# Performance work log

Hardware: AMD Instinct MI355X
Metric: run time of the kernel (lower is better)

## Reference

```python
import jax, jax.numpy as jnp
import numpy as np

DIM = 256
KEY_DIM = 16
NUM_HEADS = 8
ATTN_RATIO = 4
NH_KD = KEY_DIM * NUM_HEADS   # 128
D = ATTN_RATIO * KEY_DIM      # 64
DH = D * NUM_HEADS            # 512
POS_LEN = 16
SCALE = KEY_DIM ** -0.5


def _cbn(x, w, s, b):
    # 1x1 conv (no bias) + folded BatchNorm affine. w: [out,in], x: [B,in,H,W]
    y = jnp.einsum('oi,bihw->bohw', w, x)
    return y * s[None, :, None, None] + b[None, :, None, None]


def _interp_pos(pos, n):
    # F.interpolate(mode='linear', align_corners=False) from length POS_LEN to n.
    L = pos.shape[-1]
    coords = (jnp.arange(n, dtype=pos.dtype) + 0.5) * (L / n) - 0.5
    coords = jnp.clip(coords, 0.0, L - 1)
    lo = jnp.floor(coords).astype(jnp.int32)
    hi = jnp.minimum(lo + 1, L - 1)
    t = coords - lo.astype(pos.dtype)
    return pos[..., lo] * (1 - t) + pos[..., hi] * t  # [1,C,n]


def _axial_attn(q_emb, k_emb, v_emb, pos_q, pos_k, n):
    # q_emb/k_emb: [B,NH_KD,n], v_emb: [B,DH,n]
    B = q_emb.shape[0]
    q = (q_emb + _interp_pos(pos_q, n)).reshape(B, NUM_HEADS, KEY_DIM, n)
    k = (k_emb + _interp_pos(pos_k, n)).reshape(B, NUM_HEADS, KEY_DIM, n)
    v = v_emb.reshape(B, NUM_HEADS, D, n)
    attn = jnp.einsum('bhcn,bhcm->bhnm', q, k) * SCALE
    attn = jax.nn.softmax(attn, axis=-1)
    xx = jnp.einsum('bhnm,bhdm->bhnd', attn, v)      # [B,NH,n,D]
    return xx.transpose(0, 1, 3, 2).reshape(B, DH, n)  # [B,DH,n]


def _forward(x, wq, sq, bq, wk, sk, bk, wv, sv, bv,
             pos_rowq, pos_rowk, pos_colq, pos_colk,
             w_row, s_row, b_row, w_col, s_col, b_col,
             w_proj, s_proj, b_proj, w_sc, s_sc, b_sc,
             w_dw, s_dw, b_dw, w_pw, s_pw, b_pw):
    B, C, H, W = x.shape
    q = _cbn(x, wq, sq, bq)   # [B,NH_KD,H,W]
    k = _cbn(x, wk, sk, bk)
    v = _cbn(x, wv, sv, bv)   # [B,DH,H,W]

    # row branch (mean over W)
    xx_row = _axial_attn(q.mean(-1), k.mean(-1), v.mean(-1), pos_rowq, pos_rowk, H)
    xx_row = _cbn(jax.nn.relu(xx_row[..., None]), w_row, s_row, b_row)      # [B,DH,H,1]
    # column branch (mean over H)
    xx_col = _axial_attn(q.mean(-2), k.mean(-2), v.mean(-2), pos_colq, pos_colk, W)
    xx_col = _cbn(jax.nn.relu(xx_col[:, :, None, :]), w_col, s_col, b_col)  # [B,DH,1,W]

    attn_out = v + (xx_row + xx_col)
    attn_out = _cbn(jax.nn.relu(attn_out), w_proj, s_proj, b_proj)          # [B,DIM,H,W]

    # gate branch: 1x1 -> dw3x3 -> relu -> 1x1 -> h_sigmoid
    gate = _cbn(x, w_sc, s_sc, b_sc)
    gate = jax.lax.conv_general_dilated(
        gate, w_dw, (1, 1), 'SAME',
        dimension_numbers=('NCHW', 'OIHW', 'NCHW'), feature_group_count=DIM)
    gate = gate * s_dw[None, :, None, None] + b_dw[None, :, None, None]
    gate = jax.nn.relu(gate)
    gate = _cbn(gate, w_pw, s_pw, b_pw)
    gate = jnp.clip(gate + 3.0, 0.0, 6.0) / 6.0  # h_sigmoid
    return gate * attn_out


def setup_inputs() -> dict:
    key = jax.random.key(0)
    ks = jax.random.split(key, 32)
    B, H, W = 16, 64, 64
    nrm = lambda k, sh, sc=0.05: jax.random.normal(k, sh, dtype=jnp.float32) * sc
    inp = {
        'x': nrm(ks[0], (B, DIM, H, W), 1.0),
        'wq': nrm(ks[1], (NH_KD, DIM)), 'sq': 1.0 + nrm(ks[2], (NH_KD,)), 'bq': nrm(ks[3], (NH_KD,)),
        'wk': nrm(ks[4], (NH_KD, DIM)), 'sk': 1.0 + nrm(ks[5], (NH_KD,)), 'bk': nrm(ks[6], (NH_KD,)),
        'wv': nrm(ks[7], (DH, DIM)), 'sv': 1.0 + nrm(ks[8], (DH,)), 'bv': nrm(ks[9], (DH,)),
        'pos_rowq': nrm(ks[10], (1, NH_KD, POS_LEN), 1.0), 'pos_rowk': nrm(ks[11], (1, NH_KD, POS_LEN), 1.0),
        'pos_colq': nrm(ks[12], (1, NH_KD, POS_LEN), 1.0), 'pos_colk': nrm(ks[13], (1, NH_KD, POS_LEN), 1.0),
        'w_row': nrm(ks[14], (DH, DH)), 's_row': 1.0 + nrm(ks[15], (DH,)), 'b_row': nrm(ks[16], (DH,)),
        'w_col': nrm(ks[17], (DH, DH)), 's_col': 1.0 + nrm(ks[18], (DH,)), 'b_col': nrm(ks[19], (DH,)),
        'w_proj': nrm(ks[20], (DIM, DH)), 's_proj': 1.0 + nrm(ks[21], (DIM,)), 'b_proj': nrm(ks[22], (DIM,)),
        'w_sc': nrm(ks[23], (DIM, DIM)), 's_sc': 1.0 + nrm(ks[24], (DIM,)), 'b_sc': nrm(ks[25], (DIM,)),
        'w_dw': nrm(ks[26], (DIM, 1, 3, 3)), 's_dw': 1.0 + nrm(ks[27], (DIM,)), 'b_dw': nrm(ks[28], (DIM,)),
        'w_pw': nrm(ks[29], (DIM, DIM)), 's_pw': 1.0 + nrm(ks[30], (DIM,)), 'b_pw': nrm(ks[31], (DIM,)),
    }
    return inp


def reference(x, wq, sq, bq, wk, sk, bk, wv, sv, bv,
              pos_rowq, pos_rowk, pos_colq, pos_colk,
              w_row, s_row, b_row, w_col, s_col, b_col,
              w_proj, s_proj, b_proj, w_sc, s_sc, b_sc,
              w_dw, s_dw, b_dw, w_pw, s_pw, b_pw):
    return _forward(x, wq, sq, bq, wk, sk, bk, wv, sv, bv,
                    pos_rowq, pos_rowk, pos_colq, pos_colk,
                    w_row, s_row, b_row, w_col, s_col, b_col,
                    w_proj, s_proj, b_proj, w_sc, s_sc, b_sc,
                    w_dw, s_dw, b_dw, w_pw, s_pw, b_pw)
```

## Files before the change

kernel.cpp:

```cpp
#include <hip/hip_runtime.h>
#include <math.h>

typedef unsigned short u16;
typedef unsigned int u32;
typedef short short8 __attribute__((ext_vector_type(8)));
typedef float f32x4 __attribute__((ext_vector_type(4)));

#define Bn 16
#define Cc 256
#define Pp 4096
#define DHc 512
#define PTOT 65536
#define SCALE 0.25f

__device__ __forceinline__ float bf2f(u16 u) {
    return __uint_as_float(((u32)u) << 16);
}
__device__ __forceinline__ u16 f2bf(float f) {
    u32 u = __float_as_uint(f);
    u32 lsb = (u >> 16) & 1u;
    u += 0x7fffu + lsb;
    return (u16)(u >> 16);
}

__device__ __forceinline__ void gload16(const u16* g, u16* l) {
    __builtin_amdgcn_global_load_lds(
        (const __attribute__((address_space(1))) void*)(uintptr_t)g,
        (__attribute__((address_space(3))) void*)(u32)(uintptr_t)l,
        16, 0, 0);
}

__global__ __launch_bounds__(256) void mean_kernel(
    const float* __restrict__ x, u16* __restrict__ xmb) {
    __shared__ float plane[64][65];
    int bc = blockIdx.x;
    int b = bc >> 8, c = bc & 255;
    const float* xp = x + (size_t)bc * Pp;
    int tid = threadIdx.x;
#pragma unroll
    for (int k = 0; k < 16; ++k) {
        int idx = tid + k * 256;
        plane[idx >> 6][idx & 63] = xp[idx];
    }
    __syncthreads();
    if (tid < 64) {
        float s = 0.f;
#pragma unroll
        for (int w = 0; w < 64; ++w) s += plane[tid][w];
        xmb[((size_t)b * 64 + tid) * 256 + c] = f2bf(s * (1.f / 64.f));
    } else if (tid < 128) {
        int w = tid - 64;
        float s = 0.f;
#pragma unroll
        for (int h = 0; h < 64; ++h) s += plane[h][w];
        xmb[((size_t)1024 + b * 64 + w) * 256 + c] = f2bf(s * (1.f / 64.f));
    }
}

__global__ __launch_bounds__(256) void xpose_kernel(
    const float* __restrict__ x, u16* __restrict__ xbf) {
    __shared__ float tile[64][65];
    int pb = blockIdx.x;
    int cb = blockIdx.y;
    int b = blockIdx.z;
    int t = threadIdx.x;
    int p_l = t & 63, c_q = t >> 6;
    const float* xp = x + ((size_t)b * Cc + cb * 64) * Pp + pb * 64;
#pragma unroll
    for (int rr = 0; rr < 16; ++rr) {
        int c_l = rr * 4 + c_q;
        tile[p_l][c_l] = xp[(size_t)c_l * Pp + p_l];
    }
    __syncthreads();
    int c_l2 = t & 63, p_q = t >> 6;
    u16* dst = xbf + ((size_t)b * Pp + pb * 64) * Cc + cb * 64;
#pragma unroll
    for (int rr = 0; rr < 16; ++rr) {
        int p_l2 = rr * 4 + p_q;
        dst[(size_t)p_l2 * Cc + c_l2] = f2bf(tile[p_l2][c_l2]);
    }
}

__global__ __launch_bounds__(256) void wconv_kernel(
    const float* __restrict__ wq, const float* __restrict__ wk, const float* __restrict__ wv,
    const float* __restrict__ wsc, const float* __restrict__ wproj, const float* __restrict__ wpw,
    const float* __restrict__ wrow, const float* __restrict__ wcol,
    const float* __restrict__ wdw,
    u16* __restrict__ wqkvb, u16* __restrict__ wscb,
    u16* __restrict__ wprojb, u16* __restrict__ wpwb,
    u16* __restrict__ wrb, u16* __restrict__ wcb, float* __restrict__ wdwT) {
    int t = blockIdx.x * 256 + threadIdx.x;
    if (t < 2304) wdwT[(t % 9) * 256 + (t / 9)] = wdw[t];
    if (t < 32768) wqkvb[t] = f2bf(wq[t]);
    else if (t < 65536) wqkvb[t] = f2bf(wk[t - 32768]);
    else if (t < 196608) wqkvb[t] = f2bf(wv[t - 65536]);
    else if (t < 262144) wscb[t - 196608] = f2bf(wsc[t - 196608]);
    else if (t < 393216) wprojb[t - 262144] = f2bf(wproj[t - 262144]);
    else if (t < 458752) wpwb[t - 393216] = f2bf(wpw[t - 393216]);
    else if (t < 720896) wrb[t - 458752] = f2bf(wrow[t - 458752]);
    else wcb[t - 720896] = f2bf(wcol[t - 720896]);
}

__device__ __forceinline__ void gemm_mainloop(
    const u16* __restrict__ W, const u16* __restrict__ X, int K,
    int o0, size_t prow0, u16* ldsA, u16* ldsB, f32x4 (&acc)[4][4]) {
    int t = threadIdx.x;
    int w = t >> 6, lane = t & 63;
    int sr = (w << 5) + (lane >> 2);
    int ks = (lane & 3) * 8;
    const u16* gA = W + (size_t)(o0 + sr) * K + ks;
    const u16* gB = X + (prow0 + sr) * K + ks;
    u16* lA = ldsA + sr * 32 + ks;
    u16* lB = ldsB + sr * 32 + ks;
    int wo = (w >> 1) * 64, wp = (w & 1) * 64;
    const u16* fA = ldsA + (wo + (lane & 15)) * 32 + ((lane >> 4) * 8);
    const u16* fB = ldsB + (wp + (lane & 15)) * 32 + ((lane >> 4) * 8);

    for (int k0 = 0; k0 < K; k0 += 32) {
        if (k0) __syncthreads();
        gload16(gA + k0, lA);
        gload16(gA + k0 + (size_t)16 * K, lA + 16 * 32);
        gload16(gB + k0, lB);
        gload16(gB + k0 + (size_t)16 * K, lB + 16 * 32);
        __syncthreads();
        short8 a[4], b[4];
#pragma unroll
        for (int i = 0; i < 4; ++i) a[i] = *(const short8*)(fA + i * 16 * 32);
#pragma unroll
        for (int j = 0; j < 4; ++j) b[j] = *(const short8*)(fB + j * 16 * 32);
#pragma unroll
        for (int i = 0; i < 4; ++i)
#pragma unroll
            for (int j = 0; j < 4; ++j)
                acc[i][j] = __builtin_amdgcn_mfma_f32_16x16x32_bf16(a[i], b[j], acc[i][j], 0, 0, 0);
    }
}

__global__ __launch_bounds__(256) void gemm_qkv(
    const u16* __restrict__ Wb, const u16* __restrict__ X,
    const float* __restrict__ sq, const float* __restrict__ bq,
    const float* __restrict__ sk, const float* __restrict__ bk,
    const float* __restrict__ sv, const float* __restrict__ bv,
    const float* __restrict__ posrq, const float* __restrict__ posrk,
    const float* __restrict__ poscq, const float* __restrict__ posck,
    float* __restrict__ qrow, float* __restrict__ krow, float* __restrict__ vrow,
    float* __restrict__ qcol, float* __restrict__ kcol, float* __restrict__ vcol) {
    __shared__ u16 ldsA[128 * 32];
    __shared__ u16 ldsB[128 * 32];
    f32x4 acc[4][4];
#pragma unroll
    for (int i = 0; i < 4; ++i)
#pragma unroll
        for (int j = 0; j < 4; ++j) acc[i][j] = (f32x4){0.f, 0.f, 0.f, 0.f};
    int o0 = blockIdx.x * 128;
    size_t prow0 = (size_t)blockIdx.y * 128;
    gemm_mainloop(Wb, X, 256, o0, prow0, ldsA, ldsB, acc);

    int lane = threadIdx.x & 63, w = threadIdx.x >> 6;
    int wo = (w >> 1) * 64, wp = (w & 1) * 64;
    int quad = lane >> 4, cn = lane & 15;
#pragma unroll
    for (int j = 0; j < 4; ++j) {
        int p = (int)prow0 + wp + j * 16 + cn;
        int branch = p >> 10, loc = p & 1023;
        int b = loc >> 6, n = loc & 63;
        float coords = 0.25f * (float)n - 0.375f;
        coords = fminf(fmaxf(coords, 0.f), 15.f);
        int lo = (int)floorf(coords);
        int hi = min(lo + 1, 15);
        float tt = coords - (float)lo;
#pragma unroll
        for (int i = 0; i < 4; ++i) {
            int o = o0 + wo + i * 16 + quad * 4;
            if (o < 128) {
                const float* pos = branch ? poscq : posrq;
                float* dst = branch ? qcol : qrow;
#pragma unroll
                for (int r = 0; r < 4; ++r) {
                    int c = o + r;
                    float pv = pos[c * 16 + lo] * (1.f - tt) + pos[c * 16 + hi] * tt;
                    dst[b * 8192 + c * 64 + n] = acc[i][j][r] * sq[c] + bq[c] + pv;
                }
            } else if (o < 256) {
                const float* pos = branch ? posck : posrk;
                float* dst = branch ? kcol : krow;
#pragma unroll
                for (int r = 0; r < 4; ++r) {
                    int c = o - 128 + r;
                    float pv = pos[c * 16 + lo] * (1.f - tt) + pos[c * 16 + hi] * tt;
                    dst[b * 8192 + c * 64 + n] = acc[i][j][r] * sk[c] + bk[c] + pv;
                }
            } else {
                float* dst = branch ? vcol : vrow;
#pragma unroll
                for (int r = 0; r < 4; ++r) {
                    int c = o - 256 + r;
                    dst[b * 32768 + c * 64 + n] = acc[i][j][r] * sv[c] + bv[c];
                }
            }
        }
    }
}

__global__ __launch_bounds__(512) void attn_kernel(
    const float* __restrict__ qr, const float* __restrict__ kr, const float* __restrict__ vr,
    const float* __restrict__ qc, const float* __restrict__ kc, const float* __restrict__ vc,
    u16* __restrict__ xxbf) {
    int branch = blockIdx.y;
    const float* q = branch ? qc : qr;
    const float* k = branch ? kc : kr;
    const float* v = branch ? vc : vr;
    int bh = blockIdx.x;
    int b = bh >> 3, h = bh & 7;
    __shared__ float qs[16][64], ks[16][64], vs[64][64];
    int t = threadIdx.x;
#pragma unroll
    for (int i = t; i < 1024; i += 512) {
        int c = i >> 6, nn = i & 63;
        qs[c][nn] = q[b * 8192 + (h * 16 + c) * 64 + nn];
        ks[c][nn] = k[b * 8192 + (h * 16 + c) * 64 + nn];
    }
#pragma unroll
    for (int i = t; i < 4096; i += 512) {
        int d = i >> 6, nn = i & 63;
        vs[d][nn] = v[b * 32768 + (h * 64 + d) * 64 + nn];
    }
    __syncthreads();

    int n = t & 63, dq = t >> 6;
    float qv[16];
#pragma unroll
    for (int c = 0; c < 16; ++c) qv[c] = qs[c][n];

    float s[64];
    float mx = -1e30f;
    for (int m = 0; m < 64; ++m) {
        float acc = 0.f;
#pragma unroll
        for (int c = 0; c < 16; ++c) acc += qv[c] * ks[c][m];
        acc *= SCALE;
        s[m] = acc;
        mx = fmaxf(mx, acc);
    }
    float sum = 0.f;
    for (int m = 0; m < 64; ++m) {
        s[m] = __expf(s[m] - mx);
        sum += s[m];
    }
    float inv = 1.f / sum;
    u16* dst = xxbf + (((size_t)(b * 2 + branch)) * 64 + n) * 512 + h * 64 + dq * 8;
#pragma unroll
    for (int dd = 0; dd < 8; ++dd) {
        int d = dq * 8 + dd;
        float acc = 0.f;
#pragma unroll 8
        for (int m = 0; m < 64; ++m) acc += s[m] * vs[d][m];
        dst[dd] = f2bf(fmaxf(acc * inv, 0.f));
    }
}

__global__ __launch_bounds__(256) void post_gemm(
    const u16* __restrict__ xxbf, const u16* __restrict__ wrb, const u16* __restrict__ wcb,
    const float* __restrict__ s_row, const float* __restrict__ b_row,
    const float* __restrict__ s_col, const float* __restrict__ b_col,
    float* __restrict__ xr2, float* __restrict__ xc2) {
    __shared__ u16 ldsA[64 * 32];
    __shared__ u16 ldsB[256 * 32];
    int o0 = blockIdx.x * 256;
    int b = blockIdx.y;
    int branch = blockIdx.z;
    const u16* A = xxbf + ((size_t)(b * 2 + branch)) * 64 * 512;
    const u16* W = branch ? wcb : wrb;
    const float* ss = branch ? s_col : s_row;
    const float* bb = branch ? b_col : b_row;
    float* dst = (branch ? xc2 : xr2) + (size_t)b * 32768;

    f32x4 acc[4][4];
#pragma unroll
    for (int i = 0; i < 4; ++i)
#pragma unroll
        for (int j = 0; j < 4; ++j) acc[i][j] = (f32x4){0.f, 0.f, 0.f, 0.f};

    int t = threadIdx.x, w = t >> 6, lane = t & 63;
    int ks = (t & 3) * 8;
    const u16* gA = A + (size_t)(t >> 2) * 512 + ks;
    const u16* gB = W + (size_t)(o0 + (t >> 2)) * 512 + ks;
    u16* lA = ldsA + (t >> 2) * 32 + ks;
    u16* lB = ldsB + (t >> 2) * 32 + ks;
    const u16* fA = ldsA + (lane & 15) * 32 + ((lane >> 4) * 8);
    const u16* fB = ldsB + (w * 64 + (lane & 15)) * 32 + ((lane >> 4) * 8);

    for (int k0 = 0; k0 < 512; k0 += 32) {
        if (k0) __syncthreads();
        gload16(gA + k0, lA);
#pragma unroll
        for (int r = 0; r < 4; ++r)
            gload16(gB + k0 + (size_t)r * 64 * 512, lB + r * 64 * 32);
        __syncthreads();
        short8 a[4], bfr[4];
#pragma unroll
        for (int i = 0; i < 4; ++i) a[i] = *(const short8*)(fA + i * 16 * 32);
#pragma unroll
        for (int j = 0; j < 4; ++j) bfr[j] = *(const short8*)(fB + j * 16 * 32);
#pragma unroll
        for (int i = 0; i < 4; ++i)
#pragma unroll
            for (int j = 0; j < 4; ++j)
                acc[i][j] = __builtin_amdgcn_mfma_f32_16x16x32_bf16(a[i], bfr[j], acc[i][j], 0, 0, 0);
    }

    int quad = lane >> 4, cn = lane & 15;
#pragma unroll
    for (int i = 0; i < 4; ++i)
#pragma unroll
        for (int j = 0; j < 4; ++j) {
            int o = o0 + w * 64 + j * 16 + cn;
            float sv_ = ss[o], bv_ = bb[o];
#pragma unroll
            for (int r = 0; r < 4; ++r) {
                int n = i * 16 + quad * 4 + r;
                dst[n * 512 + o] = acc[i][j][r] * sv_ + bv_;
            }
        }
}

__global__ __launch_bounds__(256) void gemm_sc(
    const u16* __restrict__ Wb, const u16* __restrict__ X,
    const float* __restrict__ s, const float* __restrict__ bb, u16* __restrict__ outb) {
    __shared__ u16 ldsA[128 * 32];
    __shared__ u16 ldsB[128 * 32];
    f32x4 acc[4][4];
#pragma unroll
    for (int i = 0; i < 4; ++i)
#pragma unroll
        for (int j = 0; j < 4; ++j) acc[i][j] = (f32x4){0.f, 0.f, 0.f, 0.f};
    int o0 = blockIdx.x * 128;
    size_t prow0 = (size_t)blockIdx.y * 128;
    gemm_mainloop(Wb, X, 256, o0, prow0, ldsA, ldsB, acc);

    int lane = threadIdx.x & 63, w = threadIdx.x >> 6;
    int wo = (w >> 1) * 64, wp = (w & 1) * 64;
    int quad = lane >> 4, cn = lane & 15;
#pragma unroll
    for (int i = 0; i < 4; ++i) {
        int ob = o0 + wo + i * 16 + quad * 4;
        f32x4 s4 = *(const f32x4*)&s[ob];
        f32x4 b4 = *(const f32x4*)&bb[ob];
#pragma unroll
        for (int j = 0; j < 4; ++j) {
            size_t p = prow0 + wp + j * 16 + cn;
            ushort4 o4;
            o4.x = f2bf(acc[i][j][0] * s4[0] + b4[0]);
            o4.y = f2bf(acc[i][j][1] * s4[1] + b4[1]);
            o4.z = f2bf(acc[i][j][2] * s4[2] + b4[2]);
            o4.w = f2bf(acc[i][j][3] * s4[3] + b4[3]);
            *(ushort4*)&outb[p * 256 + ob] = o4;
        }
    }
}

__global__ __launch_bounds__(256) void gemm_pw(
    const u16* __restrict__ Wb, const u16* __restrict__ X,
    const float* __restrict__ s, const float* __restrict__ bb, u16* __restrict__ outb) {
    __shared__ u16 ldsA[128 * 32];
    __shared__ u16 ldsB[128 * 32];
    f32x4 acc[4][4];
#pragma unroll
    for (int i = 0; i < 4; ++i)
#pragma unroll
        for (int j = 0; j < 4; ++j) acc[i][j] = (f32x4){0.f, 0.f, 0.f, 0.f};
    int o0 = blockIdx.x * 128;
    size_t prow0 = (size_t)blockIdx.y * 128;
    gemm_mainloop(Wb, X, 256, o0, prow0, ldsA, ldsB, acc);

    int lane = threadIdx.x & 63, w = threadIdx.x >> 6;
    int wo = (w >> 1) * 64, wp = (w & 1) * 64;
    int quad = lane >> 4, cn = lane & 15;
#pragma unroll
    for (int i = 0; i < 4; ++i) {
        int ob = o0 + wo + i * 16 + quad * 4;
        f32x4 s4 = *(const f32x4*)&s[ob];
        f32x4 b4 = *(const f32x4*)&bb[ob];
#pragma unroll
        for (int j = 0; j < 4; ++j) {
            size_t p = prow0 + wp + j * 16 + cn;
            ushort4 o4;
            o4.x = f2bf(fminf(fmaxf(acc[i][j][0] * s4[0] + b4[0] + 3.f, 0.f), 6.f) * (1.f / 6.f));
            o4.y = f2bf(fminf(fmaxf(acc[i][j][1] * s4[1] + b4[1] + 3.f, 0.f), 6.f) * (1.f / 6.f));
            o4.z = f2bf(fminf(fmaxf(acc[i][j][2] * s4[2] + b4[2] + 3.f, 0.f), 6.f) * (1.f / 6.f));
            o4.w = f2bf(fminf(fmaxf(acc[i][j][3] * s4[3] + b4[3] + 3.f, 0.f), 6.f) * (1.f / 6.f));
            *(ushort4*)&outb[p * 256 + ob] = o4;
        }
    }
}

__global__ __launch_bounds__(512, 4) void fused_vproj(
    const u16* __restrict__ Wv, const u16* __restrict__ Wp,
    const u16* __restrict__ X,
    const float* __restrict__ sv, const float* __restrict__ bv,
    const float* __restrict__ xr2, const float* __restrict__ xc2,
    const float* __restrict__ sp, const float* __restrict__ bp,
    const u16* __restrict__ gate, float* __restrict__ out) {
    __shared__ u16 lds[64 * 512];

    int t = threadIdx.x;
    int lane = t & 63, w = t >> 6;
    int quad = lane >> 4, cn = lane & 15;
    int ppx = cn & 7;
    int p0 = blockIdx.x * 64;
    int bi = p0 >> 12;
    int hh = (p0 >> 6) & 63;

#pragma unroll
    for (int r = 0; r < 4; ++r) {
        int li = r * 512 + t;
        int p = li >> 5, ko = li & 31;
        gload16(X + ((size_t)(p0 + p)) * 256 + ((ko ^ (p & 7)) << 3),
                lds + (size_t)li * 8);
    }
    __syncthreads();

    f32x4 acc1[4][4];
#pragma unroll
    for (int i = 0; i < 4; ++i)
#pragma unroll
        for (int j = 0; j < 4; ++j) acc1[i][j] = (f32x4){0.f, 0.f, 0.f, 0.f};

    int ow = w * 64;
    const u16* gA0 = Wv + (size_t)(ow + cn) * 256 + quad * 8;
    const u16* gA1 = gA0 + (size_t)16 * 256;
    const u16* gA2 = gA0 + (size_t)32 * 256;
    const u16* gA3 = gA0 + (size_t)48 * 256;

    for (int k0 = 0; k0 < 256; k0 += 32) {
        int og = (k0 >> 3) + quad;
        short8 a[4], b[4];
        a[0] = *(const short8*)(gA0 + k0);
        a[1] = *(const short8*)(gA1 + k0);
        a[2] = *(const short8*)(gA2 + k0);
        a[3] = *(const short8*)(gA3 + k0);
#pragma unroll
        for (int j = 0; j < 4; ++j) {
            int pl = j * 16 + cn;
            b[j] = *(const short8*)&lds[pl * 256 + ((og ^ ppx) << 3)];
        }
#pragma unroll
        for (int i = 0; i < 4; ++i)
#pragma unroll
            for (int j = 0; j < 4; ++j)
                acc1[i][j] = __builtin_amdgcn_mfma_f32_16x16x32_bf16(a[i], b[j], acc1[i][j], 0, 0, 0);
    }

    __syncthreads();

#pragma unroll
    for (int i = 0; i < 4; ++i) {
        int ob = ow + i * 16 + quad * 4;
        f32x4 s4 = *(const f32x4*)&sv[ob];
        f32x4 b4 = *(const f32x4*)&bv[ob];
        f32x4 ra = *(const f32x4*)&xr2[(size_t)bi * 32768 + hh * 512 + ob];
#pragma unroll
        for (int j = 0; j < 4; ++j) {
            int p = j * 16 + cn;
            f32x4 ca = *(const f32x4*)&xc2[(size_t)bi * 32768 + p * 512 + ob];
            ushort4 o4;
            o4.x = f2bf(fmaxf(acc1[i][j][0] * s4[0] + b4[0] + ra[0] + ca[0], 0.f));
            o4.y = f2bf(fmaxf(acc1[i][j][1] * s4[1] + b4[1] + ra[1] + ca[1], 0.f));
            o4.z = f2bf(fmaxf(acc1[i][j][2] * s4[2] + b4[2] + ra[2] + ca[2], 0.f));
            o4.w = f2bf(fmaxf(acc1[i][j][3] * s4[3] + b4[3] + ra[3] + ca[3], 0.f));
            *(ushort4*)&lds[p * 512 + (ob ^ ((p & 7) << 3))] = o4;
        }
    }
    __syncthreads();

    f32x4 acc2[2][4];
#pragma unroll
    for (int i = 0; i < 2; ++i)
#pragma unroll
        for (int j = 0; j < 4; ++j) acc2[i][j] = (f32x4){0.f, 0.f, 0.f, 0.f};

    int o2w = w * 32;
    const u16* gP0 = Wp + (size_t)(o2w + cn) * 512 + quad * 8;
    const u16* gP1 = gP0 + (size_t)16 * 512;

    for (int k0 = 0; k0 < 512; k0 += 32) {
        short8 a2[2], b2[4];
        a2[0] = *(const short8*)(gP0 + k0);
        a2[1] = *(const short8*)(gP1 + k0);
        int kk = k0 + quad * 8;
#pragma unroll
        for (int j = 0; j < 4; ++j) {
            int p = j * 16 + cn;
            b2[j] = *(const short8*)&lds[p * 512 + (kk ^ ((p & 7) << 3))];
        }
#pragma unroll
        for (int i = 0; i < 2; ++i)
#pragma unroll
            for (int j = 0; j < 4; ++j)
                acc2[i][j] = __builtin_amdgcn_mfma_f32_16x16x32_bf16(a2[i], b2[j], acc2[i][j], 0, 0, 0);
    }

    int pl0 = p0 & 4095;
#pragma unroll
    for (int i = 0; i < 2; ++i) {
        int ob = o2w + i * 16 + quad * 4;
        f32x4 s4 = *(const f32x4*)&sp[ob];
        f32x4 b4 = *(const f32x4*)&bp[ob];
#pragma unroll
        for (int j = 0; j < 4; ++j) {
            int p = j * 16 + cn;
            size_t pg = (size_t)p0 + p;
            ushort4 gv = *(const ushort4*)&gate[pg * 256 + ob];
            float* op = out + (size_t)bi * 1048576 + (size_t)ob * 4096 + (pl0 + p);
            op[0 * 4096] = bf2f(gv.x) * (acc2[i][j][0] * s4[0] + b4[0]);
            op[1 * 4096] = bf2f(gv.y) * (acc2[i][j][1] * s4[1] + b4[1]);
            op[2 * 4096] = bf2f(gv.z) * (acc2[i][j][2] * s4[2] + b4[2]);
            op[3 * 4096] = bf2f(gv.w) * (acc2[i][j][3] * s4[3] + b4[3]);
        }
    }
}

__global__ __launch_bounds__(256) void dw_kernel(
    const u16* __restrict__ sc, const float* __restrict__ wdwT,
    const float* __restrict__ sdw, const float* __restrict__ bdw, u16* __restrict__ dwout) {
    int t = blockIdx.x * 256 + threadIdx.x;
    int cg = (t & 31) * 8;
    size_t p = (size_t)(t >> 5);
    int h = (int)((p >> 6) & 63), w_ = (int)(p & 63);
    float acc[8] = {0.f, 0.f, 0.f, 0.f, 0.f, 0.f, 0.f, 0.f};
#pragma unroll
    for (int ky = 0; ky < 3; ++ky) {
        int hh = h + ky - 1;
        if (hh < 0 || hh > 63) continue;
#pragma unroll
        for (int kx = 0; kx < 3; ++kx) {
            int wx = w_ + kx - 1;
            if (wx < 0 || wx > 63) continue;
            size_t pp = (size_t)((long long)p + (ky - 1) * 64 + (kx - 1));
            short8 v = *(const short8*)&sc[pp * 256 + cg];
            const float* wt = &wdwT[(ky * 3 + kx) * 256 + cg];
            f32x4 w0 = *(const f32x4*)wt;
            f32x4 w1 = *(const f32x4*)(wt + 4);
            acc[0] += w0[0] * bf2f((u16)v[0]); acc[1] += w0[1] * bf2f((u16)v[1]);
            acc[2] += w0[2] * bf2f((u16)v[2]); acc[3] += w0[3] * bf2f((u16)v[3]);
            acc[4] += w1[0] * bf2f((u16)v[4]); acc[5] += w1[1] * bf2f((u16)v[5]);
            acc[6] += w1[2] * bf2f((u16)v[6]); acc[7] += w1[3] * bf2f((u16)v[7]);
        }
    }
    f32x4 s0 = *(const f32x4*)&sdw[cg], s1 = *(const f32x4*)&sdw[cg + 4];
    f32x4 b0 = *(const f32x4*)&bdw[cg], b1 = *(const f32x4*)&bdw[cg + 4];
    short8 o;
    o[0] = (short)f2bf(fmaxf(acc[0] * s0[0] + b0[0], 0.f));
    o[1] = (short)f2bf(fmaxf(acc[1] * s0[1] + b0[1], 0.f));
    o[2] = (short)f2bf(fmaxf(acc[2] * s0[2] + b0[2], 0.f));
    o[3] = (short)f2bf(fmaxf(acc[3] * s0[3] + b0[3], 0.f));
    o[4] = (short)f2bf(fmaxf(acc[4] * s1[0] + b1[0], 0.f));
    o[5] = (short)f2bf(fmaxf(acc[5] * s1[1] + b1[1], 0.f));
    o[6] = (short)f2bf(fmaxf(acc[6] * s1[2] + b1[2], 0.f));
    o[7] = (short)f2bf(fmaxf(acc[7] * s1[3] + b1[3], 0.f));
    *(short8*)&dwout[p * 256 + cg] = o;
}

extern "C" void kernel_launch(void* const* d_in, const int* in_sizes, int n_in,
                              void* d_out, int out_size, void* d_ws, size_t ws_size,
                              hipStream_t stream) {
    const float* x = (const float*)d_in[0];
    const float* wq = (const float*)d_in[1];
    const float* sq = (const float*)d_in[2];
    const float* bq = (const float*)d_in[3];
    const float* wk = (const float*)d_in[4];
    const float* sk = (const float*)d_in[5];
    const float* bk = (const float*)d_in[6];
    const float* wv = (const float*)d_in[7];
    const float* sv = (const float*)d_in[8];
    const float* bv = (const float*)d_in[9];
    const float* posrq = (const float*)d_in[10];
    const float* posrk = (const float*)d_in[11];
    const float* poscq = (const float*)d_in[12];
    const float* posck = (const float*)d_in[13];
    const float* w_row = (const float*)d_in[14];
    const float* s_row = (const float*)d_in[15];
    const float* b_row = (const float*)d_in[16];
    const float* w_col = (const float*)d_in[17];
    const float* s_col = (const float*)d_in[18];
    const float* b_col = (const float*)d_in[19];
    const float* w_proj = (const float*)d_in[20];
    const float* s_proj = (const float*)d_in[21];
    const float* b_proj = (const float*)d_in[22];
    const float* w_sc = (const float*)d_in[23];
    const float* s_sc = (const float*)d_in[24];
    const float* b_sc = (const float*)d_in[25];
    const float* w_dw = (const float*)d_in[26];
    const float* s_dw = (const float*)d_in[27];
    const float* b_dw = (const float*)d_in[28];
    const float* w_pw = (const float*)d_in[29];
    const float* s_pw = (const float*)d_in[30];
    const float* b_pw = (const float*)d_in[31];
    float* out = (float*)d_out;

    float* fws = (float*)d_ws;
    float* qrow = fws;
    float* krow = qrow + 131072;
    float* qcol = krow + 131072;
    float* kcol = qcol + 131072;
    float* vrow = kcol + 131072;
    float* vcol = vrow + 524288;
    float* xr2  = vcol + 524288;
    float* xc2  = xr2 + 524288;
    float* wdwT = xc2 + 524288;
    u16* xmb    = (u16*)(wdwT + 2304);
    u16* xbf    = xmb + 524288;
    u16* wqkvb  = xbf + (size_t)PTOT * 256;
    u16* wscb   = wqkvb + 196608;
    u16* wprojb = wscb + 65536;
    u16* wpwb   = wprojb + 131072;
    u16* wrb    = wpwb + 65536;
    u16* wcb    = wrb + 262144;
    u16* xxbf   = wcb + 262144;
    u16* scb    = xxbf + 1048576;
    u16* dwb    = scb + (size_t)PTOT * 256;
    u16* gate   = scb;

    mean_kernel<<<dim3(Bn * Cc), 256, 0, stream>>>(x, xmb);
    xpose_kernel<<<dim3(64, 4, Bn), 256, 0, stream>>>(x, xbf);
    wconv_kernel<<<dim3(3840), 256, 0, stream>>>(
        wq, wk, wv, w_sc, w_proj, w_pw, w_row, w_col, w_dw,
        wqkvb, wscb, wprojb, wpwb, wrb, wcb, wdwT);
    gemm_qkv<<<dim3(6, 16), 256, 0, stream>>>(
        wqkvb, xmb, sq, bq, sk, bk, sv, bv,
        posrq, posrk, poscq, posck, qrow, krow, vrow, qcol, kcol, vcol);
    attn_kernel<<<dim3(128, 2), 512, 0, stream>>>(qrow, krow, vrow, qcol, kcol, vcol, xxbf);
    post_gemm<<<dim3(2, Bn, 2), 256, 0, stream>>>(
        xxbf, wrb, wcb, s_row, b_row, s_col, b_col, xr2, xc2);
    gemm_sc<<<dim3(2, 512), 256, 0, stream>>>(wscb, xbf, s_sc, b_sc, scb);
    dw_kernel<<<dim3(8192), 256, 0, stream>>>(scb, wdwT, s_dw, b_dw, dwb);
    gemm_pw<<<dim3(2, 512), 256, 0, stream>>>(wpwb, dwb, s_pw, b_pw, gate);
    fused_vproj<<<dim3(1024), 512, 0, stream>>>(
        wqkvb + 65536, wprojb, xbf, sv, bv, xr2, xc2, s_proj, b_proj, gate, out);
}
```

Baseline: 460.6 us.

## Shrink GEMM tiles to 32 pixels and load operands directly from global memory

Merges the shortcut and pointwise 1x1-conv GEMMs into one kernel that takes a hard-sigmoid flag. That kernel uses 512-thread blocks over 32-pixel tiles and reads A and B fragments straight from global memory instead of staging them through LDS. The fused v/proj kernel likewise halves its pixel tile to 32, drops the LDS staging of X, and launches twice as many blocks. The aim is more parallelism and less LDS and barrier overhead, at the cost of less operand reuse per block and more redundant global and L2 traffic for the weights.

```diff
diff --git a/kernel.cpp b/kernel.cpp
--- a/kernel.cpp
+++ b/kernel.cpp
@@ -324,71 +324,59 @@
         }
 }
 
-__global__ __launch_bounds__(256) void gemm_sc(
+__global__ __launch_bounds__(512, 4) void gemm_cbn256(
     const u16* __restrict__ Wb, const u16* __restrict__ X,
-    const float* __restrict__ s, const float* __restrict__ bb, u16* __restrict__ outb) {
-    __shared__ u16 ldsA[128 * 32];
-    __shared__ u16 ldsB[128 * 32];
-    f32x4 acc[4][4];
-#pragma unroll
-    for (int i = 0; i < 4; ++i)
-#pragma unroll
-        for (int j = 0; j < 4; ++j) acc[i][j] = (f32x4){0.f, 0.f, 0.f, 0.f};
-    int o0 = blockIdx.x * 128;
-    size_t prow0 = (size_t)blockIdx.y * 128;
-    gemm_mainloop(Wb, X, 256, o0, prow0, ldsA, ldsB, acc);
-
-    int lane = threadIdx.x & 63, w = threadIdx.x >> 6;
-    int wo = (w >> 1) * 64, wp = (w & 1) * 64;
+    const float* __restrict__ s, const float* __restrict__ bb,
+    u16* __restrict__ outb, int hsig) {
+    int t = threadIdx.x;
+    int lane = t & 63, w = t >> 6;
     int quad = lane >> 4, cn = lane & 15;
-#pragma unroll
-    for (int i = 0; i < 4; ++i) {
-        int ob = o0 + wo + i * 16 + quad * 4;
+    size_t p0 = (size_t)blockIdx.x * 32;
+    int o2w = w * 32;
+
+    const u16* gA0 = Wb + (size_t)(o2w + cn) * 256 + quad * 8;
+    const u16* gA1 = gA0 + (size_t)16 * 256;
+    const u16* gB0 = X + (p0 + cn) * 256 + quad * 8;
+    const u16* gB1 = gB0 + (size_t)16 * 256;
+
+    f32x4 acc[2][2];
+#pragma unroll
+    for (int i = 0; i < 2; ++i)
+#pragma unroll
+        for (int j = 0; j < 2; ++j) acc[i][j] = (f32x4){0.f, 0.f, 0.f, 0.f};
+
+#pragma unroll
+    for (int k0 = 0; k0 < 256; k0 += 32) {
+        short8 a0 = *(const short8*)(gA0 + k0);
+        short8 a1 = *(const short8*)(gA1 + k0);
+        short8 b0 = *(const short8*)(gB0 + k0);
+        short8 b1 = *(const short8*)(gB1 + k0);
+        acc[0][0] = __builtin_amdgcn_mfma_f32_16x16x32_bf16(a0, b0, acc[0][0], 0, 0, 0);
+        acc[0][1] = __builtin_amdgcn_mfma_f32_16x16x32_bf16(a0, b1, acc[0][1], 0, 0, 0);
+        acc[1][0] = __builtin_amdgcn_mfma_f32_16x16x32_bf16(a1, b0, acc[1][0], 0, 0, 0);
+        acc[1][1] = __builtin_amdgcn_mfma_f32_16x16x32_bf16(a1, b1, acc[1][1], 0, 0, 0);
+    }
+
+#pragma unroll
+    for (int i = 0; i < 2; ++i) {
+        int ob = o2w + i * 16 + quad * 4;
         f32x4 s4 = *(const f32x4*)&s[ob];
         f32x4 b4 = *(const f32x4*)&bb[ob];
 #pragma unroll
-        for (int j = 0; j < 4; ++j) {
-            size_t p = prow0 + wp + j * 16 + cn;
+        for (int j = 0; j < 2; ++j) {
+            size_t p = p0 + j * 16 + cn;
             ushort4 o4;
-            o4.x = f2bf(acc[i][j][0] * s4[0] + b4[0]);
-            o4.y = f2bf(acc[i][j][1] * s4[1] + b4[1]);
-            o4.z = f2bf(acc[i][j][2] * s4[2] + b4[2]);
-            o4.w = f2bf(acc[i][j][3] * s4[3] + b4[3]);
-            *(ushort4*)&outb[p * 256 + ob] = o4;
-        }
-    }
-}
-
-__global__ __launch_bounds__(256) void gemm_pw(
-    const u16* __restrict__ Wb, const u16* __restrict__ X,
-    const float* __restrict__ s, const float* __restrict__ bb, u16* __restrict__ outb) {
-    __shared__ u16 ldsA[128 * 32];
-    __shared__ u16 ldsB[128 * 32];
-    f32x4 acc[4][4];
-#pragma unroll
-    for (int i = 0; i < 4; ++i)
-#pragma unroll
-        for (int j = 0; j < 4; ++j) acc[i][j] = (f32x4){0.f, 0.f, 0.f, 0.f};
-    int o0 = blockIdx.x * 128;
-    size_t prow0 = (size_t)blockIdx.y * 128;
-    gemm_mainloop(Wb, X, 256, o0, prow0, ldsA, ldsB, acc);
-
-    int lane = threadIdx.x & 63, w = threadIdx.x >> 6;
-    int wo = (w >> 1) * 64, wp = (w & 1) * 64;
-    int quad = lane >> 4, cn = lane & 15;
-#pragma unroll
-    for (int i = 0; i < 4; ++i) {
-        int ob = o0 + wo + i * 16 + quad * 4;
-        f32x4 s4 = *(const f32x4*)&s[ob];
-        f32x4 b4 = *(const f32x4*)&bb[ob];
-#pragma unroll
-        for (int j = 0; j < 4; ++j) {
-            size_t p = prow0 + wp + j * 16 + cn;
-            ushort4 o4;
-            o4.x = f2bf(fminf(fmaxf(acc[i][j][0] * s4[0] + b4[0] + 3.f, 0.f), 6.f) * (1.f / 6.f));
-            o4.y = f2bf(fminf(fmaxf(acc[i][j][1] * s4[1] + b4[1] + 3.f, 0.f), 6.f) * (1.f / 6.f));
-            o4.z = f2bf(fminf(fmaxf(acc[i][j][2] * s4[2] + b4[2] + 3.f, 0.f), 6.f) * (1.f / 6.f));
-            o4.w = f2bf(fminf(fmaxf(acc[i][j][3] * s4[3] + b4[3] + 3.f, 0.f), 6.f) * (1.f / 6.f));
+            if (hsig) {
+                o4.x = f2bf(fminf(fmaxf(acc[i][j][0] * s4[0] + b4[0] + 3.f, 0.f), 6.f) * (1.f / 6.f));
+                o4.y = f2bf(fminf(fmaxf(acc[i][j][1] * s4[1] + b4[1] + 3.f, 0.f), 6.f) * (1.f / 6.f));
+                o4.z = f2bf(fminf(fmaxf(acc[i][j][2] * s4[2] + b4[2] + 3.f, 0.f), 6.f) * (1.f / 6.f));
+                o4.w = f2bf(fminf(fmaxf(acc[i][j][3] * s4[3] + b4[3] + 3.f, 0.f), 6.f) * (1.f / 6.f));
+            } else {
+                o4.x = f2bf(acc[i][j][0] * s4[0] + b4[0]);
+                o4.y = f2bf(acc[i][j][1] * s4[1] + b4[1]);
+                o4.z = f2bf(acc[i][j][2] * s4[2] + b4[2]);
+                o4.w = f2bf(acc[i][j][3] * s4[3] + b4[3]);
+            }
             *(ushort4*)&outb[p * 256 + ob] = o4;
         }
     }
@@ -401,57 +389,39 @@
     const float* __restrict__ xr2, const float* __restrict__ xc2,
     const float* __restrict__ sp, const float* __restrict__ bp,
     const u16* __restrict__ gate, float* __restrict__ out) {
-    __shared__ u16 lds[64 * 512];
+    __shared__ u16 abt[32 * 512];
 
     int t = threadIdx.x;
     int lane = t & 63, w = t >> 6;
     int quad = lane >> 4, cn = lane & 15;
-    int ppx = cn & 7;
-    int p0 = blockIdx.x * 64;
+    int p0 = blockIdx.x * 32;
     int bi = p0 >> 12;
     int hh = (p0 >> 6) & 63;
-
-#pragma unroll
-    for (int r = 0; r < 4; ++r) {
-        int li = r * 512 + t;
-        int p = li >> 5, ko = li & 31;
-        gload16(X + ((size_t)(p0 + p)) * 256 + ((ko ^ (p & 7)) << 3),
-                lds + (size_t)li * 8);
-    }
-    __syncthreads();
-
-    f32x4 acc1[4][4];
+    int w0 = p0 & 63;
+
+    f32x4 acc1[4][2];
 #pragma unroll
     for (int i = 0; i < 4; ++i)
 #pragma unroll
-        for (int j = 0; j < 4; ++j) acc1[i][j] = (f32x4){0.f, 0.f, 0.f, 0.f};
+        for (int j = 0; j < 2; ++j) acc1[i][j] = (f32x4){0.f, 0.f, 0.f, 0.f};
 
     int ow = w * 64;
-    const u16* gA0 = Wv + (size_t)(ow + cn) * 256 + quad * 8;
-    const u16* gA1 = gA0 + (size_t)16 * 256;
-    const u16* gA2 = gA0 + (size_t)32 * 256;
-    const u16* gA3 = gA0 + (size_t)48 * 256;
-
+    const u16* gA = Wv + (size_t)(ow + cn) * 256 + quad * 8;
+    const u16* gB = X + ((size_t)p0 + cn) * 256 + quad * 8;
+
+#pragma unroll
     for (int k0 = 0; k0 < 256; k0 += 32) {
-        int og = (k0 >> 3) + quad;
-        short8 a[4], b[4];
-        a[0] = *(const short8*)(gA0 + k0);
-        a[1] = *(const short8*)(gA1 + k0);
-        a[2] = *(const short8*)(gA2 + k0);
-        a[3] = *(const short8*)(gA3 + k0);
-#pragma unroll
-        for (int j = 0; j < 4; ++j) {
-            int pl = j * 16 + cn;
-            b[j] = *(const short8*)&lds[pl * 256 + ((og ^ ppx) << 3)];
-        }
+        short8 a[4], b[2];
+#pragma unroll
+        for (int i = 0; i < 4; ++i) a[i] = *(const short8*)(gA + (size_t)i * 16 * 256 + k0);
+#pragma unroll
+        for (int j = 0; j < 2; ++j) b[j] = *(const short8*)(gB + (size_t)j * 16 * 256 + k0);
 #pragma unroll
         for (int i = 0; i < 4; ++i)
 #pragma unroll
-            for (int j = 0; j < 4; ++j)
+            for (int j = 0; j < 2; ++j)
                 acc1[i][j] = __builtin_amdgcn_mfma_f32_16x16x32_bf16(a[i], b[j], acc1[i][j], 0, 0, 0);
     }
-
-    __syncthreads();
 
 #pragma unroll
     for (int i = 0; i < 4; ++i) {
@@ -460,43 +430,43 @@
         f32x4 b4 = *(const f32x4*)&bv[ob];
         f32x4 ra = *(const f32x4*)&xr2[(size_t)bi * 32768 + hh * 512 + ob];
 #pragma unroll
-        for (int j = 0; j < 4; ++j) {
+        for (int j = 0; j < 2; ++j) {
             int p = j * 16 + cn;
-            f32x4 ca = *(const f32x4*)&xc2[(size_t)bi * 32768 + p * 512 + ob];
+            f32x4 ca = *(const f32x4*)&xc2[(size_t)bi * 32768 + (w0 + p) * 512 + ob];
             ushort4 o4;
             o4.x = f2bf(fmaxf(acc1[i][j][0] * s4[0] + b4[0] + ra[0] + ca[0], 0.f));
             o4.y = f2bf(fmaxf(acc1[i][j][1] * s4[1] + b4[1] + ra[1] + ca[1], 0.f));
             o4.z = f2bf(fmaxf(acc1[i][j][2] * s4[2] + b4[2] + ra[2] + ca[2], 0.f));
             o4.w = f2bf(fmaxf(acc1[i][j][3] * s4[3] + b4[3] + ra[3] + ca[3], 0.f));
-            *(ushort4*)&lds[p * 512 + (ob ^ ((p & 7) << 3))] = o4;
+            *(ushort4*)&abt[p * 512 + (ob ^ ((p & 7) << 3))] = o4;
         }
     }
     __syncthreads();
 
-    f32x4 acc2[2][4];
+    f32x4 acc2[2][2];
 #pragma unroll
     for (int i = 0; i < 2; ++i)
 #pragma unroll
-        for (int j = 0; j < 4; ++j) acc2[i][j] = (f32x4){0.f, 0.f, 0.f, 0.f};
+        for (int j = 0; j < 2; ++j) acc2[i][j] = (f32x4){0.f, 0.f, 0.f, 0.f};
 
     int o2w = w * 32;
-    const u16* gP0 = Wp + (size_t)(o2w + cn) * 512 + quad * 8;
-    const u16* gP1 = gP0 + (size_t)16 * 512;
-
+    const u16* gP = Wp + (size_t)(o2w + cn) * 512 + quad * 8;
+
+#pragma unroll
     for (int k0 = 0; k0 < 512; k0 += 32) {
-        short8 a2[2], b2[4];
-        a2[0] = *(const short8*)(gP0 + k0);
-        a2[1] = *(const short8*)(gP1 + k0);
+        short8 a2[2], b2[2];
+#pragma unroll
+        for (int i = 0; i < 2; ++i) a2[i] = *(const short8*)(gP + (size_t)i * 16 * 512 + k0);
         int kk = k0 + quad * 8;
 #pragma unroll
-        for (int j = 0; j < 4; ++j) {
+        for (int j = 0; j < 2; ++j) {
             int p = j * 16 + cn;
-            b2[j] = *(const short8*)&lds[p * 512 + (kk ^ ((p & 7) << 3))];
+            b2[j] = *(const short8*)&abt[p * 512 + (kk ^ ((p & 7) << 3))];
         }
 #pragma unroll
         for (int i = 0; i < 2; ++i)
 #pragma unroll
-            for (int j = 0; j < 4; ++j)
+            for (int j = 0; j < 2; ++j)
                 acc2[i][j] = __builtin_amdgcn_mfma_f32_16x16x32_bf16(a2[i], b2[j], acc2[i][j], 0, 0, 0);
     }
 
@@ -507,7 +477,7 @@
         f32x4 s4 = *(const f32x4*)&sp[ob];
         f32x4 b4 = *(const f32x4*)&bp[ob];
 #pragma unroll
-        for (int j = 0; j < 4; ++j) {
+        for (int j = 0; j < 2; ++j) {
             int p = j * 16 + cn;
             size_t pg = (size_t)p0 + p;
             ushort4 gv = *(const ushort4*)&gate[pg * 256 + ob];
@@ -632,9 +602,9 @@
     attn_kernel<<<dim3(128, 2), 512, 0, stream>>>(qrow, krow, vrow, qcol, kcol, vcol, xxbf);
     post_gemm<<<dim3(2, Bn, 2), 256, 0, stream>>>(
         xxbf, wrb, wcb, s_row, b_row, s_col, b_col, xr2, xc2);
-    gemm_sc<<<dim3(2, 512), 256, 0, stream>>>(wscb, xbf, s_sc, b_sc, scb);
+    gemm_cbn256<<<dim3(2048), 512, 0, stream>>>(wscb, xbf, s_sc, b_sc, scb, 0);
     dw_kernel<<<dim3(8192), 256, 0, stream>>>(scb, wdwT, s_dw, b_dw, dwb);
-    gemm_pw<<<dim3(2, 512), 256, 0, stream>>>(wpwb, dwb, s_pw, b_pw, gate);
-    fused_vproj<<<dim3(1024), 512, 0, stream>>>(
+    gemm_cbn256<<<dim3(2048), 512, 0, stream>>>(wpwb, dwb, s_pw, b_pw, gate, 1);
+    fused_vproj<<<dim3(2048), 512, 0, stream>>>(
         wqkvb + 65536, wprojb, xbf, sv, bv, xr2, xc2, s_proj, b_proj, gate, out);
 }
```

Result: slower. 600.1 us (+30.3%).
